# Kernel tuning notes

Hardware: AMD Instinct MI355X
Metric: run time of the kernel (lower is better)

The kernel has to match this reference:

```python
import jax, jax.numpy as jnp
import numpy as np

B, T, D, N, K, H = 2, 2048, 2048, 16, 8, 128
WINDOW = 1024
SOFT_CAP = 50.0
Q_SCALE = H ** -0.5  # query_pre_attn_scalar
ROPE_BASE = 10000
ROPE_SCALE = 1.0
K_MASK = -2.3819763e38


def apply_rope(x, positions, base_frequency=ROPE_BASE, scale_factor=ROPE_SCALE):
    # x: [B, T, n, H], positions: [B, T]
    head_dim = x.shape[-1]
    fraction = 2.0 * jnp.arange(head_dim // 2, dtype=jnp.float32) / head_dim
    timescale = base_frequency ** fraction  # [H/2]
    sin_inp = positions[..., None].astype(jnp.float32) / timescale  # [B,T,H/2]
    sin_inp = sin_inp[..., None, :] / scale_factor  # [B,T,1,H/2]
    sin, cos = jnp.sin(sin_inp), jnp.cos(sin_inp)
    x1, x2 = jnp.split(x, 2, axis=-1)
    out = jnp.concatenate([x1 * cos - x2 * sin, x2 * cos + x1 * sin], axis=-1)
    return out.astype(x.dtype)


def rms_norm(x, scale, eps=1e-6):
    var = jnp.mean(jnp.square(x.astype(jnp.float32)), axis=-1, keepdims=True)
    normed = x * jax.lax.rsqrt(var + eps)
    return (normed * (1.0 + scale)).astype(x.dtype)


def setup_inputs() -> dict:
    key = jax.random.key(0)
    ks = jax.random.split(key, 4)
    x = jax.random.normal(ks[0], (B, T, D), jnp.float32)
    segment_pos = jnp.tile(jnp.arange(T, dtype=jnp.int32)[None, :], (B, 1))
    attn_mask = jnp.tril(jnp.ones((T, T), dtype=bool))[None].repeat(B, axis=0)
    w_q = jax.random.normal(ks[1], (N, D, H), jnp.float32) * (D ** -0.5)
    w_kv = jax.random.normal(ks[2], (2, K, D, H), jnp.float32) * (D ** -0.5)
    w_o = jax.random.normal(ks[3], (N, H, D), jnp.float32) * ((N * H) ** -0.5)
    q_norm_scale = jnp.zeros((H,), jnp.float32)
    k_norm_scale = jnp.zeros((H,), jnp.float32)
    return dict(x=x, w_q=w_q, w_kv=w_kv, w_o=w_o,
                q_norm_scale=q_norm_scale, k_norm_scale=k_norm_scale,
                segment_pos=segment_pos, attn_mask=attn_mask)


def reference(x, w_q, w_kv, w_o, q_norm_scale, k_norm_scale, segment_pos, attn_mask):
    # projections
    q = jnp.einsum('BTD,NDH->BTNH', x, w_q)              # [B,T,N,H]
    kv = jnp.einsum('BSD,CKDH->CBSKH', x, w_kv)          # [2,B,S,K,H]
    k, v = kv[0], kv[1]
    # QK RMSNorm
    q = rms_norm(q, q_norm_scale)
    k = rms_norm(k, k_norm_scale)
    # RoPE + query scaling
    q = apply_rope(q, segment_pos) * Q_SCALE
    k = apply_rope(k, segment_pos)
    # GQA logits
    G = N // K
    qg = q.reshape(B, T, K, G, H)
    logits = jnp.einsum('BTKGH,BSKH->BTKGS', qg, k).reshape(B, T, N, T)
    # soft cap
    logits = jnp.tanh(logits / SOFT_CAP) * SOFT_CAP
    # sliding-window mask combined with causal attn_mask
    pos_q = segment_pos[:, :, None]
    pos_k = segment_pos[:, None, :]
    sliding = (pos_k > pos_q - WINDOW) & (pos_k < pos_q + WINDOW)
    mask = attn_mask & sliding                           # [B,T,S]
    padded = jnp.where(mask[:, :, None, :], logits, K_MASK)
    probs = jax.nn.softmax(padded, axis=-1).astype(k.dtype)
    # GQA weighted values
    enc = jnp.einsum('BTKGS,BSKH->BTKGH', probs.reshape(B, T, K, G, T), v)
    enc = enc.reshape(B, T, N, H)
    # split/concat of navigator vs scribe heads is an identity on output
    return jnp.einsum('BTNH,NHD->BTD', enc, w_o)
```

## Files before the change

### kernel.cpp

```cpp
#include <hip/hip_runtime.h>
#include <stdint.h>

typedef __attribute__((ext_vector_type(8))) short short8;
typedef __attribute__((ext_vector_type(4))) float f32x4;

#define B_ 2
#define T_ 2048
#define D_ 2048
#define N_ 16
#define KH_ 8
#define H_ 128
#define WINDOW_ 1024

__device__ __forceinline__ uint16_t f2bf(float f) {
  union { float f; uint32_t u; } a; a.f = f;
  uint32_t u = a.u;
  return (uint16_t)((u + 0x7FFFu + ((u >> 16) & 1u)) >> 16);
}

__device__ __forceinline__ void gl_lds16(const void* g, void* l) {
  __builtin_amdgcn_global_load_lds((const __attribute__((address_space(1))) void*)g,
                                   (__attribute__((address_space(3))) void*)l, 16, 0, 0);
}

__global__ __launch_bounds__(256) void k_f2b4(const float* __restrict__ src,
                                              uint16_t* __restrict__ dst, long n) {
  long i = ((long)blockIdx.x * 256 + threadIdx.x) * 4;
  if (i >= n) return;
  float4 v = *(const float4*)(src + i);
  uint64_t p = (uint64_t)f2bf(v.x) | ((uint64_t)f2bf(v.y) << 16) |
               ((uint64_t)f2bf(v.z) << 32) | ((uint64_t)f2bf(v.w) << 48);
  *(uint64_t*)(dst + i) = p;
}

__global__ __launch_bounds__(256)
void k_transpose_f2b(const float* __restrict__ src, uint16_t* __restrict__ dst,
                     int R, int C, int nb1, long sbs1, long sbs2, long dbs,
                     long src_off, int srs) {
  __shared__ float tile[32][33];
  int z = blockIdx.z;
  int b1 = z % nb1, b2 = z / nb1;
  const float* s = src + src_off + (long)b1 * sbs1 + (long)b2 * sbs2;
  uint16_t* d = dst + (long)z * dbs;
  int c0 = blockIdx.x * 32, r0 = blockIdx.y * 32;
  int x = threadIdx.x, y = threadIdx.y;
#pragma unroll
  for (int j = 0; j < 4; ++j)
    tile[y + j * 8][x] = s[(long)(r0 + y + j * 8) * srs + (c0 + x)];
  __syncthreads();
#pragma unroll
  for (int j = 0; j < 4; ++j)
    d[(long)(c0 + y + j * 8) * R + (r0 + x)] = f2bf(tile[x][y + j * 8]);
}

__global__ __launch_bounds__(256)
void k_transpose_v(const float* __restrict__ kvg, uint16_t* __restrict__ vbt) {
  __shared__ float tile[32][33];
  int z = blockIdx.z;
  int kh = z % KH_, b = z / KH_;
  const float* s = kvg + (long)b * T_ * 2048 + 1024 + kh * H_;
  uint16_t* d = vbt + (long)z * H_ * T_;
  int h0 = blockIdx.x * 32, s0 = blockIdx.y * 32;
  int x = threadIdx.x, y = threadIdx.y;
#pragma unroll
  for (int j = 0; j < 4; ++j)
    tile[y + j * 8][x] = s[(long)(s0 + y + j * 8) * 2048 + (h0 + x)];
  __syncthreads();
#pragma unroll
  for (int j = 0; j < 4; ++j) {
    int h = h0 + y + j * 8;
    int si = s0 + x;
    int ss = (si & ~63) | ((((si >> 3) & 7) ^ (h & 7)) << 3) | (si & 7);
    d[(long)h * T_ + ss] = f2bf(tile[x][y + j * 8]);
  }
}

__global__ __launch_bounds__(512, 2)
void k_gemm8(const uint16_t* __restrict__ A, const uint16_t* __restrict__ Bt,
             float* __restrict__ C0, float* __restrict__ C1, int nbx, int splitc) {
  __shared__ __align__(16) uint16_t Ls[2][2][2][128 * 64];
  int tid = threadIdx.x, lane = tid & 63, w = tid >> 6;
  int wm = w >> 2, wn = w & 3;
  int fr = lane & 15, fgrp = lane >> 4;
  int bid = blockIdx.x;
  int k2 = bid >> 3;
  long by = (bid & 7) * 2 + k2 / nbx;
  long bx = k2 % nbx;
  long row0 = by * 256, col0 = bx * 256;

  int trow = tid >> 3;
  int kse = (((tid & 7) * 16) ^ ((trow & 7) << 4)) >> 1;
  const uint16_t* aS[2] = { A + (row0 + trow) * 2048 + kse,
                            A + (row0 + 128 + trow) * 2048 + kse };
  const uint16_t* bS[2] = { Bt + (col0 + trow) * 2048 + kse,
                            Bt + (col0 + 128 + trow) * 2048 + kse };
  char* ldsbase = (char*)Ls + w * 1024;

  int kx[2] = { (fgrp * 16) ^ ((fr & 7) << 4), (64 + fgrp * 16) ^ ((fr & 7) << 4) };
  int aoffb = (wm * 64 + fr) * 128;
  int boffb = (wn * 32 + fr) * 128;
  const char* LA = (const char*)Ls;
  const char* LB = LA + 65536;

  f32x4 acc[2][2][4][2];
#pragma unroll
  for (int qm = 0; qm < 2; ++qm)
#pragma unroll
    for (int qn = 0; qn < 2; ++qn)
#pragma unroll
      for (int m = 0; m < 4; ++m)
#pragma unroll
        for (int n = 0; n < 2; ++n) acc[qm][qn][m][n] = (f32x4){0.f, 0.f, 0.f, 0.f};

#define STG(MAT, SLOT, HALF, KT) do {                                      \
    const uint16_t* _g = (MAT ? bS[HALF] : aS[HALF]) + (KT) * 64;          \
    char* _l = ldsbase + (MAT) * 65536 + (SLOT) * 32768 + (HALF) * 16384;  \
    gl_lds16(_g, _l);                                                      \
    gl_lds16(_g + 64 * 2048, _l + 8192);                                   \
  } while (0)

#define PH(SLOT, QM, QN, STMT, VM) do {                                               \
    short8 _a[4][2], _b[2][2];                                                        \
    _Pragma("unroll") for (int m = 0; m < 4; ++m) {                                   \
      _a[m][0] = *(const short8*)(LA + (SLOT)*32768 + (QM)*16384 + aoffb + m*2048 + kx[0]); \
      _a[m][1] = *(const short8*)(LA + (SLOT)*32768 + (QM)*16384 + aoffb + m*2048 + kx[1]); } \
    _Pragma("unroll") for (int n = 0; n < 2; ++n) {                                   \
      _b[n][0] = *(const short8*)(LB + (SLOT)*32768 + (QN)*16384 + boffb + n*2048 + kx[0]); \
      _b[n][1] = *(const short8*)(LB + (SLOT)*32768 + (QN)*16384 + boffb + n*2048 + kx[1]); } \
    STMT;                                                                             \
    __builtin_amdgcn_s_barrier();                                                     \
    asm volatile("s_waitcnt lgkmcnt(0)" ::: "memory");                                \
    __builtin_amdgcn_sched_barrier(0);                                                \
    __builtin_amdgcn_s_setprio(1);                                                    \
    _Pragma("unroll") for (int m = 0; m < 4; ++m)                                     \
      _Pragma("unroll") for (int n = 0; n < 2; ++n) {                                 \
        acc[QM][QN][m][n] = __builtin_amdgcn_mfma_f32_16x16x32_bf16(_a[m][0], _b[n][0], acc[QM][QN][m][n], 0, 0, 0); \
        acc[QM][QN][m][n] = __builtin_amdgcn_mfma_f32_16x16x32_bf16(_a[m][1], _b[n][1], acc[QM][QN][m][n], 0, 0, 0); } \
    __builtin_amdgcn_s_setprio(0);                                                    \
    if (VM) { asm volatile("s_waitcnt vmcnt(4)" ::: "memory");                        \
              __builtin_amdgcn_sched_barrier(0); }                                    \
    __builtin_amdgcn_s_barrier();                                                     \
    __builtin_amdgcn_sched_barrier(0);                                                \
  } while (0)

  STG(0, 0, 0, 0); STG(1, 0, 0, 0); STG(1, 0, 1, 0); STG(0, 0, 1, 0);
  STG(0, 1, 0, 1); STG(1, 1, 0, 1);
  asm volatile("s_waitcnt vmcnt(4)" ::: "memory");
  __builtin_amdgcn_sched_barrier(0);
  __builtin_amdgcn_s_barrier();

#pragma unroll 1
  for (int it = 0; it < 16; ++it) {
    int t1 = 2 * it + 1, t2 = (2 * it + 2) & 31, t3 = (2 * it + 3) & 31;
    PH(0, 0, 0, STG(1, 1, 1, t1), 0);
    PH(0, 0, 1, STG(0, 1, 1, t1), 0);
    PH(0, 1, 0, STG(0, 0, 0, t2), 0);
    PH(0, 1, 1, STG(1, 0, 0, t2), 1);
    PH(1, 0, 0, STG(1, 0, 1, t2), 0);
    PH(1, 0, 1, STG(0, 0, 1, t2), 0);
    PH(1, 1, 0, STG(0, 1, 0, t3), 0);
    PH(1, 1, 1, STG(1, 1, 0, t3), 1);
  }
#undef PH
#undef STG

  int og = fgrp * 4;
  bool hic = (col0 >= splitc);
  float* Cb = hic ? C1 : C0;
  long cb = col0 - (hic ? splitc : 0);
#pragma unroll
  for (int qm = 0; qm < 2; ++qm)
#pragma unroll
    for (int qn = 0; qn < 2; ++qn)
#pragma unroll
      for (int m = 0; m < 4; ++m)
#pragma unroll
        for (int n = 0; n < 2; ++n) {
          long r = row0 + qm * 128 + wm * 64 + m * 16 + og;
          long c = cb + qn * 128 + wn * 32 + n * 16 + fr;
          float* cp = Cb + r * 2048 + c;
#pragma unroll
          for (int i = 0; i < 4; ++i) cp[(long)i * 2048] = acc[qm][qn][m][n][i];
        }
}

__global__ __launch_bounds__(256)
void k_qpost(const float* __restrict__ qg, const float* __restrict__ qs,
             uint16_t* __restrict__ qb) {
  int gw = blockIdx.x * 4 + (threadIdx.x >> 6);
  int lane = threadIdx.x & 63;
  int bt = gw / N_;
  int t = bt % T_;
  const float* src = qg + (long)gw * H_;
  float x1 = src[lane], x2 = src[lane + 64];
  float ssq = x1 * x1 + x2 * x2;
#pragma unroll
  for (int off = 1; off < 64; off <<= 1) ssq += __shfl_xor(ssq, off);
  float inv = rsqrtf(ssq * (1.0f / 128.0f) + 1e-6f);
  float n1 = x1 * inv * (1.0f + qs[lane]);
  float n2 = x2 * inv * (1.0f + qs[lane + 64]);
  float ts = powf(10000.0f, (float)lane * (2.0f / 128.0f));
  float ang = (float)t / ts;
  float sn, cs;
  sincosf(ang, &sn, &cs);
  const float QSC = 0.08838834764831845f;
  uint16_t* dp = qb + (long)gw * H_;
  dp[lane] = f2bf((n1 * cs - n2 * sn) * QSC);
  dp[lane + 64] = f2bf((n2 * cs + n1 * sn) * QSC);
}

__global__ __launch_bounds__(256)
void k_kpost(const float* __restrict__ kvg, const float* __restrict__ ks,
             uint16_t* __restrict__ kb) {
  int gw = blockIdx.x * 4 + (threadIdx.x >> 6);
  int lane = threadIdx.x & 63;
  int kh = gw % KH_;
  int bt = gw / KH_;
  int t = bt % T_, b = bt / T_;
  const float* src = kvg + (long)bt * (KH_ * H_ * 2) + kh * H_;
  float x1 = src[lane], x2 = src[lane + 64];
  float ssq = x1 * x1 + x2 * x2;
#pragma unroll
  for (int off = 1; off < 64; off <<= 1) ssq += __shfl_xor(ssq, off);
  float inv = rsqrtf(ssq * (1.0f / 128.0f) + 1e-6f);
  float n1 = x1 * inv * (1.0f + ks[lane]);
  float n2 = x2 * inv * (1.0f + ks[lane + 64]);
  float ts = powf(10000.0f, (float)lane * (2.0f / 128.0f));
  float ang = (float)t / ts;
  float sn, cs;
  sincosf(ang, &sn, &cs);
  int sw = (t & 7) << 3;
  uint16_t* dp = kb + ((long)(b * KH_ + kh) * T_ + t) * H_;
  dp[lane ^ sw] = f2bf(n1 * cs - n2 * sn);
  dp[(lane + 64) ^ sw] = f2bf(n2 * cs + n1 * sn);
}

__global__ __launch_bounds__(256, 4)
void k_attn(const uint16_t* __restrict__ qb, const uint16_t* __restrict__ kb,
            const uint16_t* __restrict__ vbt, uint16_t* __restrict__ enc) {
  __shared__ uint16_t Ks[64 * 128];
  __shared__ uint16_t Vs[128 * 64];
  __shared__ uint16_t Pl[4][16 * 64];
  int tid = threadIdx.x, lane = tid & 63, w = tid >> 6;
  int nt = T_ / 64;
  int blk = blockIdx.x;
  int tq = nt - 1 - (blk >> 5);
  int bn = blk & 31;
  int n = bn % N_, b = bn / N_;
  int kh = n >> 1;
  int t0 = tq * 64;
  int tw = t0 + w * 16;
  int fr = lane & 15, fgrp = lane >> 4, fk = fgrp * 8;
  int sw3 = fr & 7;
  const float M0 = 20.0f;

  const uint16_t* qrow = qb + ((long)(b * T_ + tw + fr) * N_ + n) * H_;
  short8 aq[4];
#pragma unroll
  for (int kk = 0; kk < 4; ++kk) aq[kk] = *(const short8*)(qrow + kk * 32 + fk);

  float lrow[4];
  f32x4 o[8];
#pragma unroll
  for (int i = 0; i < 4; ++i) lrow[i] = 0.0f;
#pragma unroll
  for (int hf = 0; hf < 8; ++hf) o[hf] = (f32x4){0.f, 0.f, 0.f, 0.f};

  int s_begin = t0 - (WINDOW_ - 1);
  if (s_begin < 0) s_begin = 0;
  s_begin &= ~63;
  int s_endex = t0 + 64;

  const uint16_t* kbase = kb + (long)(b * KH_ + kh) * T_ * H_;
  const uint16_t* vbase = vbt + (long)(b * KH_ + kh) * H_ * T_;
  int krow_st = tid >> 4, kcol_st = (tid & 15) * 8;
  int vrow_st = tid >> 3, vcol_st = (tid & 7) * 8;
  char* ldsK = (char*)Ks + w * 1024;
  char* ldsV = (char*)Vs + w * 1024;
  uint16_t* Pw = Pl[w];

  for (int s0 = s_begin; s0 < s_endex; s0 += 64) {
    __syncthreads();
#pragma unroll
    for (int j = 0; j < 4; ++j) {
      gl_lds16(kbase + (long)(s0 + j * 16 + krow_st) * H_ + kcol_st, ldsK + j * 4096);
      gl_lds16(vbase + (long)(j * 32 + vrow_st) * T_ + s0 + vcol_st, ldsV + j * 4096);
    }
    __syncthreads();
    if (s0 > tw + 15 || s0 + 63 < tw - (WINDOW_ - 1)) continue;

    f32x4 sc[4];
#pragma unroll
    for (int kc = 0; kc < 4; ++kc) {
      f32x4 a = (f32x4){0.f, 0.f, 0.f, 0.f};
      const uint16_t* kr = Ks + (kc * 16 + fr) * 128;
#pragma unroll
      for (int kk = 0; kk < 4; ++kk) {
        short8 bk = *(const short8*)(kr + ((((kk << 2) | fgrp) ^ sw3) << 3));
        a = __builtin_amdgcn_mfma_f32_16x16x32_bf16(aq[kk], bk, a, 0, 0, 0);
      }
      sc[kc] = a;
    }

    bool full = (s0 + 63 <= tw) && (s0 >= tw + 16 - WINDOW_);
    if (full) {
#pragma unroll
      for (int i = 0; i < 4; ++i)
#pragma unroll
        for (int kc = 0; kc < 4; ++kc) {
          float v = sc[kc][i];
          sc[kc][i] = 50.0f - 100.0f / (__expf(v * 0.04f) + 1.0f);
        }
    } else {
#pragma unroll
      for (int i = 0; i < 4; ++i) {
        int trow = tw + fgrp * 4 + i;
#pragma unroll
        for (int kc = 0; kc < 4; ++kc) {
          int s = s0 + kc * 16 + fr;
          float v = sc[kc][i];
          float c = 50.0f - 100.0f / (__expf(v * 0.04f) + 1.0f);
          bool ok = (s <= trow) && (s > trow - WINDOW_);
          sc[kc][i] = ok ? c : -1e30f;
        }
      }
    }

#pragma unroll
    for (int i = 0; i < 4; ++i) {
      int r = fgrp * 4 + i;
      int rsw = (r & 7) << 3;
      float ps = 0.f;
#pragma unroll
      for (int kc = 0; kc < 4; ++kc) {
        float p = __expf(sc[kc][i] - M0);
        ps += p;
        Pw[r * 64 + ((kc * 16 + fr) ^ rsw)] = f2bf(p);
      }
      lrow[i] += ps;
    }

    short8 pa0 = *(const short8*)(Pw + fr * 64 + ((fgrp ^ sw3) << 3));
    short8 pa1 = *(const short8*)(Pw + fr * 64 + (((4 | fgrp) ^ sw3) << 3));
#pragma unroll
    for (int hf = 0; hf < 8; ++hf) {
      const uint16_t* vr = Vs + (hf * 16 + fr) * 64;
      short8 bv0 = *(const short8*)(vr + ((fgrp ^ sw3) << 3));
      short8 bv1 = *(const short8*)(vr + (((4 | fgrp) ^ sw3) << 3));
      o[hf] = __builtin_amdgcn_mfma_f32_16x16x32_bf16(pa0, bv0, o[hf], 0, 0, 0);
      o[hf] = __builtin_amdgcn_mfma_f32_16x16x32_bf16(pa1, bv1, o[hf], 0, 0, 0);
    }
  }

#pragma unroll
  for (int i = 0; i < 4; ++i) {
#pragma unroll
    for (int off = 1; off < 16; off <<= 1) lrow[i] += __shfl_xor(lrow[i], off);
    lrow[i] = 1.0f / lrow[i];
  }
#pragma unroll
  for (int hf = 0; hf < 8; ++hf)
#pragma unroll
    for (int i = 0; i < 4; ++i) {
      int t = tw + fgrp * 4 + i;
      float val = o[hf][i] * lrow[i];
      enc[((long)(b * T_ + t) * N_ + n) * H_ + hf * 16 + fr] = f2bf(val);
    }
}

extern "C" void kernel_launch(void* const* d_in, const int* in_sizes, int n_in,
                              void* d_out, int out_size, void* d_ws, size_t ws_size,
                              hipStream_t stream) {
  const float* x = (const float*)d_in[0];
  const float* w_q = (const float*)d_in[1];
  const float* w_kv = (const float*)d_in[2];
  const float* w_o = (const float*)d_in[3];
  const float* qns = (const float*)d_in[4];
  const float* kns = (const float*)d_in[5];
  float* out = (float*)d_out;

  uint16_t* ws = (uint16_t*)d_ws;
  uint16_t* xb    = ws;
  uint16_t* wq_t  = xb    + 8388608;
  uint16_t* wkv_t = wq_t  + 4194304;
  uint16_t* wo_t  = wkv_t + 4194304;
  uint16_t* qb    = wo_t  + 4194304;
  uint16_t* kb    = qb    + 8388608;
  uint16_t* vbt   = kb    + 4194304;
  uint16_t* enc   = vbt   + 4194304;
  float* kvg = (float*)(enc + 8388608);
  if (ws_size < (size_t)125829120) return;

  dim3 tb(32, 8);
  k_f2b4<<<8192, 256, 0, stream>>>(x, xb, 8388608);
  k_transpose_f2b<<<dim3(4, 64, 16), tb, 0, stream>>>(w_q, wq_t, 2048, 128, 16,
      (long)D_ * H_, 0, (long)H_ * D_, 0, H_);
  k_transpose_f2b<<<dim3(4, 64, 8), tb, 0, stream>>>(w_kv, wkv_t, 2048, 128, 8,
      (long)D_ * H_, 0, (long)H_ * D_, 0, H_);
  k_transpose_f2b<<<dim3(4, 64, 8), tb, 0, stream>>>(w_kv, wkv_t + 1024 * 2048, 2048, 128, 8,
      (long)D_ * H_, 0, (long)H_ * D_, (long)KH_ * D_ * H_, H_);
  k_transpose_f2b<<<dim3(64, 64, 1), tb, 0, stream>>>(w_o, wo_t, 2048, 2048, 1,
      0, 0, 0, 0, 2048);
  k_gemm8<<<256, 512, 0, stream>>>(xb, wq_t, out, kvg, 16, 2048);
  k_qpost<<<(B_ * T_ * N_) / 4, 256, 0, stream>>>(out, qns, qb);
  k_kpost<<<(B_ * T_ * KH_) / 4, 256, 0, stream>>>(kvg, kns, kb);
  k_transpose_v<<<dim3(4, 64, 16), tb, 0, stream>>>(kvg, vbt);
  k_attn<<<B_ * N_ * (T_ / 64), 256, 0, stream>>>(qb, kb, vbt, enc);
  k_gemm8<<<128, 512, 0, stream>>>(enc, wo_t, out, out, 8, 1 << 30);
}
```

Baseline: 264.7 us.

## Add narrower-tile output GEMM and replace softcap tanh with odd polynomial

Measured after the change: 234.5 us. 11.4% less time.

```diff
diff --git a/kernel.cpp b/kernel.cpp
--- a/kernel.cpp
+++ b/kernel.cpp
@@ -184,6 +184,111 @@
         }
 }
 
+__global__ __launch_bounds__(512, 2)
+void k_gemm8n(const uint16_t* __restrict__ A, const uint16_t* __restrict__ Bt,
+              float* __restrict__ C, int nbx) {
+  __shared__ __align__(16) uint16_t LsA[2][2][128 * 64];
+  __shared__ __align__(16) uint16_t LsB[2][128 * 64];
+  int tid = threadIdx.x, lane = tid & 63, w = tid >> 6;
+  int wm = w >> 2, wn = w & 3;
+  int fr = lane & 15, fgrp = lane >> 4;
+  int bid = blockIdx.x;
+  int k2 = bid >> 3;
+  long by = (bid & 7) * 2 + k2 / nbx;
+  long bx = k2 % nbx;
+  long row0 = by * 256, col0 = bx * 128;
+
+  int trow = tid >> 3;
+  int kse = (((tid & 7) * 16) ^ ((trow & 7) << 4)) >> 1;
+  const uint16_t* aS[2] = { A + (row0 + trow) * 2048 + kse,
+                            A + (row0 + 128 + trow) * 2048 + kse };
+  const uint16_t* bS = Bt + (col0 + trow) * 2048 + kse;
+  char* ldsA_w = (char*)LsA + w * 1024;
+  char* ldsB_w = (char*)LsB + w * 1024;
+
+  int kx[2] = { (fgrp * 16) ^ ((fr & 7) << 4), (64 + fgrp * 16) ^ ((fr & 7) << 4) };
+  int aoffb = (wm * 64 + fr) * 128;
+  int boffb = (wn * 32 + fr) * 128;
+  const char* LA = (const char*)LsA;
+  const char* LB = (const char*)LsB;
+
+  f32x4 acc[2][4][2];
+#pragma unroll
+  for (int qm = 0; qm < 2; ++qm)
+#pragma unroll
+    for (int m = 0; m < 4; ++m)
+#pragma unroll
+      for (int n = 0; n < 2; ++n) acc[qm][m][n] = (f32x4){0.f, 0.f, 0.f, 0.f};
+
+#define STGA(SLOT, HALF, KT) do {                                \
+    const uint16_t* _g = aS[HALF] + (KT) * 64;                   \
+    char* _l = ldsA_w + (SLOT) * 32768 + (HALF) * 16384;         \
+    gl_lds16(_g, _l);                                            \
+    gl_lds16(_g + 64 * 2048, _l + 8192);                         \
+  } while (0)
+#define STGB(SLOT, KT) do {                                      \
+    const uint16_t* _g = bS + (KT) * 64;                         \
+    char* _l = ldsB_w + (SLOT) * 16384;                          \
+    gl_lds16(_g, _l);                                            \
+    gl_lds16(_g + 64 * 2048, _l + 8192);                         \
+  } while (0)
+
+#define PHN(SLOT, QM, STMT, VM) do {                                                  \
+    short8 _a[4][2], _b[2][2];                                                        \
+    _Pragma("unroll") for (int m = 0; m < 4; ++m) {                                   \
+      _a[m][0] = *(const short8*)(LA + (SLOT)*32768 + (QM)*16384 + aoffb + m*2048 + kx[0]); \
+      _a[m][1] = *(const short8*)(LA + (SLOT)*32768 + (QM)*16384 + aoffb + m*2048 + kx[1]); } \
+    _Pragma("unroll") for (int n = 0; n < 2; ++n) {                                   \
+      _b[n][0] = *(const short8*)(LB + (SLOT)*16384 + boffb + n*2048 + kx[0]);        \
+      _b[n][1] = *(const short8*)(LB + (SLOT)*16384 + boffb + n*2048 + kx[1]); }      \
+    STMT;                                                                             \
+    __builtin_amdgcn_s_barrier();                                                     \
+    asm volatile("s_waitcnt lgkmcnt(0)" ::: "memory");                                \
+    __builtin_amdgcn_sched_barrier(0);                                                \
+    __builtin_amdgcn_s_setprio(1);                                                    \
+    _Pragma("unroll") for (int m = 0; m < 4; ++m)                                     \
+      _Pragma("unroll") for (int n = 0; n < 2; ++n) {                                 \
+        acc[QM][m][n] = __builtin_amdgcn_mfma_f32_16x16x32_bf16(_a[m][0], _b[n][0], acc[QM][m][n], 0, 0, 0); \
+        acc[QM][m][n] = __builtin_amdgcn_mfma_f32_16x16x32_bf16(_a[m][1], _b[n][1], acc[QM][m][n], 0, 0, 0); } \
+    __builtin_amdgcn_s_setprio(0);                                                    \
+    if (VM) { asm volatile("s_waitcnt vmcnt(2)" ::: "memory");                        \
+              __builtin_amdgcn_sched_barrier(0); }                                    \
+    __builtin_amdgcn_s_barrier();                                                     \
+    __builtin_amdgcn_sched_barrier(0);                                                \
+  } while (0)
+
+  STGA(0, 0, 0); STGA(0, 1, 0); STGB(0, 0); STGA(1, 0, 1);
+  asm volatile("s_waitcnt vmcnt(2)" ::: "memory");
+  __builtin_amdgcn_sched_barrier(0);
+  __builtin_amdgcn_s_barrier();
+
+#pragma unroll 1
+  for (int it = 0; it < 16; ++it) {
+    int t1 = 2 * it + 1, t2 = (2 * it + 2) & 31, t3 = (2 * it + 3) & 31;
+    PHN(0, 0, { STGA(1, 1, t1); STGB(1, t1); }, 0);
+    PHN(0, 1, STGA(0, 0, t2), 1);
+    PHN(1, 0, { STGA(0, 1, t2); STGB(0, t2); }, 0);
+    PHN(1, 1, STGA(1, 0, t3), 1);
+  }
+#undef PHN
+#undef STGA
+#undef STGB
+
+  int og = fgrp * 4;
+#pragma unroll
+  for (int qm = 0; qm < 2; ++qm)
+#pragma unroll
+    for (int m = 0; m < 4; ++m)
+#pragma unroll
+      for (int n = 0; n < 2; ++n) {
+        long r = row0 + qm * 128 + wm * 64 + m * 16 + og;
+        long c = col0 + wn * 32 + n * 16 + fr;
+        float* cp = C + r * 2048 + c;
+#pragma unroll
+        for (int i = 0; i < 4; ++i) cp[(long)i * 2048] = acc[qm][m][n][i];
+      }
+}
+
 __global__ __launch_bounds__(256)
 void k_qpost(const float* __restrict__ qg, const float* __restrict__ qs,
              uint16_t* __restrict__ qb) {
@@ -252,7 +357,6 @@
   int tw = t0 + w * 16;
   int fr = lane & 15, fgrp = lane >> 4, fk = fgrp * 8;
   int sw3 = fr & 7;
-  const float M0 = 20.0f;
 
   const uint16_t* qrow = qb + ((long)(b * T_ + tw + fr) * N_ + n) * H_;
   short8 aq[4];
@@ -303,42 +407,32 @@
     }
 
     bool full = (s0 + 63 <= tw) && (s0 >= tw + 16 - WINDOW_);
-    if (full) {
-#pragma unroll
-      for (int i = 0; i < 4; ++i)
-#pragma unroll
-        for (int kc = 0; kc < 4; ++kc) {
-          float v = sc[kc][i];
-          sc[kc][i] = 50.0f - 100.0f / (__expf(v * 0.04f) + 1.0f);
-        }
-    } else {
-#pragma unroll
-      for (int i = 0; i < 4; ++i) {
-        int trow = tw + fgrp * 4 + i;
-#pragma unroll
-        for (int kc = 0; kc < 4; ++kc) {
-          int s = s0 + kc * 16 + fr;
-          float v = sc[kc][i];
-          float c = 50.0f - 100.0f / (__expf(v * 0.04f) + 1.0f);
-          bool ok = (s <= trow) && (s > trow - WINDOW_);
-          sc[kc][i] = ok ? c : -1e30f;
-        }
-      }
+#define SMBODY(FULL)                                                              \
+    _Pragma("unroll") for (int i = 0; i < 4; ++i) {                               \
+      int r = fgrp * 4 + i;                                                       \
+      int rsw = (r & 7) << 3;                                                     \
+      int trowq = tw + r;                                                         \
+      float ps = 0.f;                                                             \
+      _Pragma("unroll") for (int kc = 0; kc < 4; ++kc) {                          \
+        float v = sc[kc][i];                                                      \
+        float xx = v * 0.02f;                                                     \
+        xx = fminf(1.0f, fmaxf(-1.0f, xx));                                       \
+        float u = xx * xx;                                                        \
+        float tt = xx * fmaf(u, fmaf(u, fmaf(u, -0.053968254f, 0.13333334f),      \
+                                     -0.33333334f), 1.0f);                        \
+        float p = __expf(fmaf(tt, 50.0f, -20.0f));                                \
+        if (!(FULL)) {                                                            \
+          int s = s0 + kc * 16 + fr;                                              \
+          bool ok = (s <= trowq) && (s > trowq - WINDOW_);                        \
+          p = ok ? p : 0.0f;                                                      \
+        }                                                                         \
+        ps += p;                                                                  \
+        Pw[r * 64 + ((kc * 16 + fr) ^ rsw)] = f2bf(p);                            \
+      }                                                                           \
+      lrow[i] += ps;                                                              \
     }
-
-#pragma unroll
-    for (int i = 0; i < 4; ++i) {
-      int r = fgrp * 4 + i;
-      int rsw = (r & 7) << 3;
-      float ps = 0.f;
-#pragma unroll
-      for (int kc = 0; kc < 4; ++kc) {
-        float p = __expf(sc[kc][i] - M0);
-        ps += p;
-        Pw[r * 64 + ((kc * 16 + fr) ^ rsw)] = f2bf(p);
-      }
-      lrow[i] += ps;
-    }
+    if (full) { SMBODY(true) } else { SMBODY(false) }
+#undef SMBODY
 
     short8 pa0 = *(const short8*)(Pw + fr * 64 + ((fgrp ^ sw3) << 3));
     short8 pa1 = *(const short8*)(Pw + fr * 64 + (((4 | fgrp) ^ sw3) << 3));
@@ -406,5 +500,5 @@
   k_kpost<<<(B_ * T_ * KH_) / 4, 256, 0, stream>>>(kvg, kns, kb);
   k_transpose_v<<<dim3(4, 64, 16), tb, 0, stream>>>(kvg, vbt);
   k_attn<<<B_ * N_ * (T_ / 64), 256, 0, stream>>>(qb, kb, vbt, enc);
-  k_gemm8<<<128, 512, 0, stream>>>(enc, wo_t, out, out, 8, 1 << 30);
-}
+  k_gemm8n<<<256, 512, 0, stream>>>(enc, wo_t, out, 16);
+}
```
